# Kernel optimization log

Measured on AMD Instinct MI355X. Metric: run time of the kernel, lower is better.

The kernel has to match this reference:

```python
import jax, jax.numpy as jnp
import numpy as np

B, S, D = 4, 512, 4096
H, G = 32, 8           # num_heads, num_groups (GQA)
HD = D // H            # head_dim = 128
REP = H // G           # query heads per kv group = 4


def rotate_half(x):
    x1, x2 = x[..., : x.shape[-1] // 2], x[..., x.shape[-1] // 2 :]
    return jnp.concatenate([-x2, x1], axis=-1)


def setup_inputs() -> dict:
    key = jax.random.key(0)
    ks = jax.random.split(key, 5)
    return {
        "x": jax.random.normal(ks[0], (B, S, D), dtype=jnp.float32),
        "wq": jax.random.normal(ks[1], (D, D), dtype=jnp.float32) * 0.02,
        "bq": jnp.zeros((D,), dtype=jnp.float32),
        "wk": jax.random.normal(ks[2], (D, G * HD), dtype=jnp.float32) * 0.02,
        "bk": jnp.zeros((G * HD,), dtype=jnp.float32),
        "wv": jax.random.normal(ks[3], (D, G * HD), dtype=jnp.float32) * 0.02,
        "bv": jnp.zeros((G * HD,), dtype=jnp.float32),
        "wo": jax.random.normal(ks[4], (D, D), dtype=jnp.float32) * 0.02,
        "bo": jnp.zeros((D,), dtype=jnp.float32),
    }


def reference(x, wq, bq, wk, bk, wv, bv, wo, bo):
    b, s, d = x.shape
    q = (x @ wq + bq).reshape(b, s, H, HD)
    k = (x @ wk + bk).reshape(b, s, G, HD)
    v = (x @ wv + bv).reshape(b, s, G, HD)

    # RoPE tables (identical to module's cached sin/cos, sliced to seq len)
    inv_freq = 1.0 / (10000.0 ** (jnp.arange(0, HD, 2, dtype=jnp.float32) / HD))
    freqs = jnp.outer(jnp.arange(s, dtype=jnp.float32), inv_freq)  # [s, HD/2]
    freqs = jnp.concatenate([freqs, freqs], axis=-1)               # [s, HD]
    sin = jnp.sin(freqs)[:, None, :]  # [s, 1, HD] broadcast over heads
    cos = jnp.cos(freqs)[:, None, :]

    q = q * cos + rotate_half(q) * sin
    k = k * cos + rotate_half(k) * sin

    # Module scales q by HD**-0.5 AND jax.nn.dot_product_attention applies its
    # own default 1/sqrt(HD) -> net logit scale is HD**-1. Reproduce exactly.
    scale = HD ** (-0.5)
    q = q * scale

    # GQA without materializing repeated k/v: group query heads.
    qg = q.reshape(b, s, G, REP, HD)
    logits = jnp.einsum("bqgrd,bkgd->bgrqk", qg, k) * scale  # second scale (SDPA default)
    attn = jax.nn.softmax(logits, axis=-1)
    out = jnp.einsum("bgrqk,bkgd->bqgrd", attn, v).reshape(b, s, d)
    return out @ wo + bo
```

## Files before the change

### kernel.cpp

```cpp
#include <hip/hip_runtime.h>
#include <math.h>

typedef unsigned short ushort_t;
typedef __attribute__((ext_vector_type(8))) short bf16x8;
typedef __attribute__((ext_vector_type(4))) float f32x4;
typedef __attribute__((ext_vector_type(4))) unsigned short us4;
typedef __attribute__((ext_vector_type(8))) unsigned short us8;

#define B_   4
#define S_   512
#define D_   4096
#define H_   32
#define G_   8
#define HD_  128
#define KV_  1024
#define M_   (B_ * S_)
#define QN_  6144

__device__ __forceinline__ float bf2f(ushort_t u) {
    union { unsigned u; float f; } x; x.u = ((unsigned)u) << 16; return x.f;
}
__device__ __forceinline__ ushort_t f2bf(float f) {
    union { float f; unsigned u; } x; x.f = f;
    unsigned r = x.u + 0x7fffu + ((x.u >> 16) & 1u);
    return (ushort_t)(r >> 16);
}

typedef const __attribute__((address_space(1))) void* gptr_t;
typedef __attribute__((address_space(3))) void* ldsptr_t;

__device__ __forceinline__ void gload_lds16(const void* g, void* lds) {
    __builtin_amdgcn_global_load_lds((gptr_t)g, (ldsptr_t)lds, 16, 0, 0);
}

#define BAR() asm volatile("s_barrier" ::: "memory")
#define LGKM0() do { asm volatile("s_waitcnt lgkmcnt(0)" ::: "memory"); \
                     __builtin_amdgcn_sched_barrier(0); } while (0)

__global__ void xconv(const float* __restrict__ x, ushort_t* __restrict__ xb, int n8)
{
    const int i = blockIdx.x * blockDim.x + threadIdx.x;
    if (i >= n8) return;
    const float4 a = *(const float4*)&x[(size_t)i * 8];
    const float4 b = *(const float4*)&x[(size_t)i * 8 + 4];
    us8 o;
    o[0] = f2bf(a.x); o[1] = f2bf(a.y); o[2] = f2bf(a.z); o[3] = f2bf(a.w);
    o[4] = f2bf(b.x); o[5] = f2bf(b.y); o[6] = f2bf(b.z); o[7] = f2bf(b.w);
    *(us8*)&xb[(size_t)i * 8] = o;
}

__global__ __launch_bounds__(256) void wconv_all(
    const float* __restrict__ wq, const float* __restrict__ wk,
    const float* __restrict__ wv, ushort_t* __restrict__ Wt)
{
    __shared__ float t[32][33];
    const int n0 = blockIdx.x * 32, k0 = blockIdx.y * 32;
    const float* W; int nsrc, N;
    if (n0 < 4096)      { W = wq; nsrc = n0;        N = 4096; }
    else if (n0 < 5120) { W = wk; nsrc = n0 - 4096; N = 1024; }
    else                { W = wv; nsrc = n0 - 5120; N = 1024; }
    const int tid = threadIdx.x;
    const int r = tid >> 3, c4 = (tid & 7) * 4;
    const float4 v = *(const float4*)&W[(size_t)(k0 + r) * N + nsrc + c4];
    t[r][c4 + 0] = v.x; t[r][c4 + 1] = v.y; t[r][c4 + 2] = v.z; t[r][c4 + 3] = v.w;
    __syncthreads();
    us4 o;
    o.x = f2bf(t[c4 + 0][r]);
    o.y = f2bf(t[c4 + 1][r]);
    o.z = f2bf(t[c4 + 2][r]);
    o.w = f2bf(t[c4 + 3][r]);
    *(us4*)&Wt[(size_t)(n0 + r) * D_ + k0 + c4] = o;
}

__global__ __launch_bounds__(256) void wconv(
    const float* __restrict__ W, ushort_t* __restrict__ Wt, int K, int N)
{
    __shared__ float t[32][33];
    const int n0 = blockIdx.x * 32, k0 = blockIdx.y * 32;
    const int tid = threadIdx.x;
    const int r = tid >> 3, c4 = (tid & 7) * 4;
    const float4 v = *(const float4*)&W[(size_t)(k0 + r) * N + n0 + c4];
    t[r][c4 + 0] = v.x; t[r][c4 + 1] = v.y; t[r][c4 + 2] = v.z; t[r][c4 + 3] = v.w;
    __syncthreads();
    us4 o;
    o.x = f2bf(t[c4 + 0][r]);
    o.y = f2bf(t[c4 + 1][r]);
    o.z = f2bf(t[c4 + 2][r]);
    o.w = f2bf(t[c4 + 3][r]);
    *(us4*)&Wt[(size_t)(n0 + r) * K + k0 + c4] = o;
}

template<int OUT_BF16, int SPLITK, int ROPE>
__global__ __launch_bounds__(512, 2) void gemm8(
    const ushort_t* __restrict__ A, int lda,
    const ushort_t* __restrict__ Bt, int ldb,
    const float* __restrict__ bias0, const float* __restrict__ bias1,
    const float* __restrict__ bias2,
    float* __restrict__ Cf, ushort_t* __restrict__ Cb,
    float* __restrict__ P0, float* __restrict__ P1,
    int M, int N, int K)
{
    __shared__ ushort_t sA[2][256 * 64];
    __shared__ ushort_t sB[2][256 * 64];

    const int tid = threadIdx.x;
    const int lane = tid & 63, w = tid >> 6;
    const int lr = lane & 15, kg = lane >> 4;
    const int wr = w >> 2, wc = w & 3;

    const int nwg = gridDim.x;
    const int cpx = nwg >> 3;
    const int bid = (blockIdx.x & 7) * cpx + (blockIdx.x >> 3);
    int khalf = 0, tile = bid;
    if (SPLITK) { khalf = bid >> 7; tile = bid & 127; }
    const int nbx = N >> 8;
    const int bx = tile % nbx, by = tile / nbx;
    const int bm0 = by << 8, bn0 = bx << 8;
    if (SPLITK) { A += (size_t)khalf * K; Bt += (size_t)khalf * K; }

    const int NT = K >> 6;

    auto stage = [&](int t, int h) {
        const int c = t & 1;
        const ushort_t* gb; int ld; char* sbase;
        if (h < 2) { gb = A + (size_t)bm0 * lda; ld = lda; sbase = (char*)sA; }
        else       { gb = Bt + (size_t)bn0 * ldb; ld = ldb; sbase = (char*)sB; }
        const int half = h & 1;
        #pragma unroll
        for (int j = 0; j < 2; ++j) {
            const int o = j * 8192 + tid * 16;
            const int row = half * 128 + (o >> 7);
            const int slot = (o >> 4) & 7;
            gload_lds16(gb + (size_t)row * ld + t * 64 + ((slot ^ (row & 7)) << 3),
                        sbase + c * 32768 + half * 16384 + j * 8192 + w * 1024);
        }
    };
    auto lda_frag = [&](int c, int mi, int s) {
        const int row = mi * 32 + wr * 16 + lr;
        return *(const bf16x8*)((const char*)sA + c * 32768 + row * 128 +
                                (((s * 4 + kg) ^ (row & 7)) << 4));
    };
    auto ldb_frag = [&](int c, int ni, int s) {
        const int row = ni * 64 + wc * 16 + lr;
        return *(const bf16x8*)((const char*)sB + c * 32768 + row * 128 +
                                (((s * 4 + kg) ^ (row & 7)) << 4));
    };

    f32x4 acc[8][4];
    #pragma unroll
    for (int i = 0; i < 8; ++i)
        #pragma unroll
        for (int j = 0; j < 4; ++j)
            acc[i][j] = (f32x4){0.f, 0.f, 0.f, 0.f};

    stage(0, 0); stage(0, 2); stage(0, 3); stage(0, 1);
    stage(1, 0); stage(1, 2); stage(1, 3);
    asm volatile("s_waitcnt vmcnt(6)" ::: "memory");
    BAR();

    for (int t = 0; t < NT; ++t) {
        const int c = t & 1;
        bf16x8 a[4][2], b[4][2];

        #pragma unroll
        for (int mi = 0; mi < 4; ++mi)
            #pragma unroll
            for (int s = 0; s < 2; ++s) a[mi][s] = lda_frag(c, mi, s);
        #pragma unroll
        for (int ni = 0; ni < 2; ++ni)
            #pragma unroll
            for (int s = 0; s < 2; ++s) b[ni][s] = ldb_frag(c, ni, s);
        if (t + 1 < NT) stage(t + 1, 1);
        BAR();
        LGKM0();
        __builtin_amdgcn_s_setprio(1);
        #pragma unroll
        for (int mi = 0; mi < 4; ++mi)
            #pragma unroll
            for (int ni = 0; ni < 2; ++ni)
                #pragma unroll
                for (int s = 0; s < 2; ++s)
                    acc[mi][ni] = __builtin_amdgcn_mfma_f32_16x16x32_bf16(
                        a[mi][s], b[ni][s], acc[mi][ni], 0, 0, 0);
        __builtin_amdgcn_s_setprio(0);
        BAR();

        #pragma unroll
        for (int ni = 2; ni < 4; ++ni)
            #pragma unroll
            for (int s = 0; s < 2; ++s) b[ni][s] = ldb_frag(c, ni, s);
        if (t + 2 < NT) stage(t + 2, 0);
        BAR();
        LGKM0();
        __builtin_amdgcn_s_setprio(1);
        #pragma unroll
        for (int mi = 0; mi < 4; ++mi)
            #pragma unroll
            for (int ni = 2; ni < 4; ++ni)
                #pragma unroll
                for (int s = 0; s < 2; ++s)
                    acc[mi][ni] = __builtin_amdgcn_mfma_f32_16x16x32_bf16(
                        a[mi][s], b[ni][s], acc[mi][ni], 0, 0, 0);
        __builtin_amdgcn_s_setprio(0);
        BAR();

        #pragma unroll
        for (int mi = 0; mi < 4; ++mi)
            #pragma unroll
            for (int s = 0; s < 2; ++s) a[mi][s] = lda_frag(c, mi + 4, s);
        if (t + 2 < NT) stage(t + 2, 2);
        BAR();
        LGKM0();
        __builtin_amdgcn_s_setprio(1);
        #pragma unroll
        for (int mi = 0; mi < 4; ++mi)
            #pragma unroll
            for (int ni = 2; ni < 4; ++ni)
                #pragma unroll
                for (int s = 0; s < 2; ++s)
                    acc[mi + 4][ni] = __builtin_amdgcn_mfma_f32_16x16x32_bf16(
                        a[mi][s], b[ni][s], acc[mi + 4][ni], 0, 0, 0);
        __builtin_amdgcn_s_setprio(0);
        BAR();

        if (t + 2 < NT) {
            stage(t + 2, 3);
            asm volatile("s_waitcnt vmcnt(6)" ::: "memory");
        } else {
            asm volatile("s_waitcnt vmcnt(0)" ::: "memory");
        }
        BAR();
        __builtin_amdgcn_s_setprio(1);
        #pragma unroll
        for (int mi = 0; mi < 4; ++mi)
            #pragma unroll
            for (int ni = 0; ni < 2; ++ni)
                #pragma unroll
                for (int s = 0; s < 2; ++s)
                    acc[mi + 4][ni] = __builtin_amdgcn_mfma_f32_16x16x32_bf16(
                        a[mi][s], b[ni][s], acc[mi + 4][ni], 0, 0, 0);
        __builtin_amdgcn_s_setprio(0);
        BAR();
    }

    if (ROPE && bn0 < 5120) {
        const float scale = (bn0 < 4096) ? (1.f / 128.f) : 1.f;
        const int jj = wc * 16 + lr;
        const float invf = __expf(-0.1439115683121279f * (float)jj);
        #pragma unroll
        for (int mi = 0; mi < 8; ++mi) {
            const int mr = bm0 + mi * 32 + wr * 16 + kg * 4;
            #pragma unroll
            for (int r = 0; r < 4; ++r) {
                const int srow = (mr + r) & 511;
                float sn, cs;
                __sincosf((float)srow * invf, &sn, &cs);
                #pragma unroll
                for (int nip = 0; nip < 2; ++nip) {
                    const int n_lo = bn0 + nip * 128 + jj;
                    const int n_hi = n_lo + 64;
                    const float b_lo = (n_lo < 4096) ? bias0[n_lo]
                                     : (n_lo < 5120) ? bias1[n_lo - 4096] : bias2[n_lo - 5120];
                    const float b_hi = (n_hi < 4096) ? bias0[n_hi]
                                     : (n_hi < 5120) ? bias1[n_hi - 4096] : bias2[n_hi - 5120];
                    const float a_lo = acc[mi][nip * 2][r] + b_lo;
                    const float a_hi = acc[mi][nip * 2 + 1][r] + b_hi;
                    Cb[(size_t)(mr + r) * N + n_lo] = f2bf((a_lo * cs - a_hi * sn) * scale);
                    Cb[(size_t)(mr + r) * N + n_hi] = f2bf((a_hi * cs + a_lo * sn) * scale);
                }
            }
        }
        return;
    }
    #pragma unroll
    for (int mi = 0; mi < 8; ++mi) {
        #pragma unroll
        for (int ni = 0; ni < 4; ++ni) {
            const int n = bn0 + ni * 64 + wc * 16 + lr;
            const float bs = (n < 4096) ? bias0[n]
                           : (n < 5120) ? bias1[n - 4096] : bias2[n - 5120];
            const int mr = bm0 + mi * 32 + wr * 16 + kg * 4;
            #pragma unroll
            for (int r = 0; r < 4; ++r) {
                if (SPLITK) {
                    const int row = mr + r;
                    if (khalf == 0) {
                        Cf[(size_t)row * N + n] = acc[mi][ni][r] + bs;
                    } else {
                        float* P = (row < 1024) ? P0 : P1;
                        P[((size_t)(row & 1023) << 12) + n] = acc[mi][ni][r];
                    }
                } else {
                    const float val = acc[mi][ni][r] + bs;
                    if (OUT_BF16) Cb[(size_t)(mr + r) * N + n] = f2bf(val);
                    else          Cf[(size_t)(mr + r) * N + n] = val;
                }
            }
        }
    }
}

__global__ void reduce_add(const float* __restrict__ P0, const float* __restrict__ P1,
                           float* __restrict__ out)
{
    const int n4 = M_ * D_ / 4;
    for (int i4 = blockIdx.x * blockDim.x + threadIdx.x; i4 < n4;
         i4 += gridDim.x * blockDim.x) {
        const float4 p = (i4 < (1 << 20))
            ? *(const float4*)&P0[(size_t)i4 * 4]
            : *(const float4*)&P1[(size_t)(i4 - (1 << 20)) * 4];
        float4 o = *(float4*)&out[(size_t)i4 * 4];
        o.x += p.x; o.y += p.y; o.z += p.z; o.w += p.w;
        *(float4*)&out[(size_t)i4 * 4] = o;
    }
}

__global__ __launch_bounds__(256) void vtrans(
    const ushort_t* __restrict__ vb,
    ushort_t* __restrict__ vT)
{
    __shared__ ushort_t t[32][40];
    const int s0 = blockIdx.x * 32;
    const int d0 = blockIdx.y * 32;
    const int bg = blockIdx.z;
    const int b = bg >> 3, g = bg & 7;
    const int tid = threadIdx.x;
    const int row = tid >> 3, c4 = (tid & 7) * 4;
    const us4 v = *(const us4*)&vb[(size_t)(b * S_ + s0 + row) * QN_ + g * HD_ + d0 + c4];
    t[row][c4 + 0] = v.x; t[row][c4 + 1] = v.y;
    t[row][c4 + 2] = v.z; t[row][c4 + 3] = v.w;
    __syncthreads();
    us4 o;
    o.x = t[c4 + 0][row]; o.y = t[c4 + 1][row];
    o.z = t[c4 + 2][row]; o.w = t[c4 + 3][row];
    *(us4*)&vT[(size_t)(bg * HD_ + d0 + row) * S_ + s0 + c4] = o;
}

__global__ __launch_bounds__(256) void attn_mfma(
    const ushort_t* __restrict__ kb,
    const ushort_t* __restrict__ vT,
    ushort_t* __restrict__ qb)
{
    __shared__ ushort_t sKV[8192];
    __shared__ ushort_t sP[4 * 16 * 512];

    const int q0 = blockIdx.x * 64;
    const int h = blockIdx.y, b = blockIdx.z;
    const int g = h >> 2;
    const int tid = threadIdx.x;
    const int lane = tid & 63, w = tid >> 6;
    const int lr = lane & 15, kg = lane >> 4;

    bf16x8 af[4];
    {
        const ushort_t* qrow = qb + (size_t)(b * S_ + q0 + w * 16 + lr) * QN_ + h * HD_;
        #pragma unroll
        for (int c = 0; c < 4; ++c)
            af[c] = *(const bf16x8*)(qrow + c * 32 + kg * 8);
    }

    f32x4 l[8][4];
    #pragma unroll
    for (int ch = 0; ch < 8; ++ch)
        #pragma unroll
        for (int t = 0; t < 4; ++t)
            l[ch][t] = (f32x4){0.f, 0.f, 0.f, 0.f};

    const ushort_t* kbase = kb + (size_t)b * S_ * QN_ + g * HD_;
    #pragma unroll
    for (int ch = 0; ch < 8; ++ch) {
        __syncthreads();
        #pragma unroll
        for (int i = 0; i < 4; ++i) {
            const int o = w * 4096 + i * 1024;
            const int key = (o >> 8) + (lane >> 4);
            const int sl = lane & 15;
            gload_lds16(kbase + (size_t)(ch * 64 + key) * QN_ + ((sl ^ (key & 15)) * 8),
                        (char*)sKV + o);
        }
        __syncthreads();
        #pragma unroll
        for (int t = 0; t < 4; ++t) {
            const int key = t * 16 + lr;
            #pragma unroll
            for (int c = 0; c < 4; ++c) {
                const bf16x8 bf = *(const bf16x8*)((const char*)sKV + key * 256 +
                                                   (((c * 4 + kg) ^ (key & 15)) << 4));
                l[ch][t] = __builtin_amdgcn_mfma_f32_16x16x32_bf16(af[c], bf, l[ch][t], 0, 0, 0);
            }
        }
    }

    float inv[4];
    #pragma unroll
    for (int r = 0; r < 4; ++r) {
        float m = -1e30f;
        #pragma unroll
        for (int ch = 0; ch < 8; ++ch)
            #pragma unroll
            for (int t = 0; t < 4; ++t)
                m = fmaxf(m, l[ch][t][r]);
        #pragma unroll
        for (int msk = 1; msk <= 8; msk <<= 1)
            m = fmaxf(m, __shfl_xor(m, msk));
        float s = 0.f;
        const int q = kg * 4 + r;
        #pragma unroll
        for (int ch = 0; ch < 8; ++ch)
            #pragma unroll
            for (int t = 0; t < 4; ++t) {
                const float p = __expf(l[ch][t][r] - m);
                s += p;
                const int gs = ch * 8 + t * 2 + (lr >> 3);
                sP[w * 8192 + q * 512 + ((gs ^ q) << 3) + (lr & 7)] = f2bf(p);
            }
        #pragma unroll
        for (int msk = 1; msk <= 8; msk <<= 1)
            s += __shfl_xor(s, msk);
        inv[r] = 1.f / s;
    }

    f32x4 oacc[8];
    #pragma unroll
    for (int dt = 0; dt < 8; ++dt) oacc[dt] = (f32x4){0.f, 0.f, 0.f, 0.f};

    const ushort_t* vbase = vT + (size_t)(b * G_ + g) * HD_ * S_;
    for (int ch = 0; ch < 8; ++ch) {
        __syncthreads();
        #pragma unroll
        for (int i = 0; i < 4; ++i) {
            const int o = w * 4096 + i * 1024;
            const int d = (o >> 7) + (lane >> 3);
            const int sl = lane & 7;
            gload_lds16(vbase + (size_t)d * S_ + ch * 64 + ((sl ^ (d & 7)) * 8),
                        (char*)sKV + o);
        }
        __syncthreads();
        #pragma unroll
        for (int c2 = 0; c2 < 2; ++c2) {
            const int gs = ch * 8 + c2 * 4 + kg;
            const bf16x8 ap = *(const bf16x8*)((const char*)sP + w * 16384 + lr * 1024 +
                                               ((gs ^ lr) << 4));
            #pragma unroll
            for (int dt = 0; dt < 8; ++dt) {
                const int d = dt * 16 + lr;
                const bf16x8 bv = *(const bf16x8*)((const char*)sKV + d * 128 +
                                                   (((c2 * 4 + kg) ^ (d & 7)) << 4));
                oacc[dt] = __builtin_amdgcn_mfma_f32_16x16x32_bf16(ap, bv, oacc[dt], 0, 0, 0);
            }
        }
    }

    #pragma unroll
    for (int dt = 0; dt < 8; ++dt) {
        #pragma unroll
        for (int r = 0; r < 4; ++r) {
            const int q = kg * 4 + r;
            qb[(size_t)(b * S_ + q0 + w * 16 + q) * QN_ + h * HD_ + dt * 16 + lr] =
                f2bf(oacc[dt][r] * inv[r]);
        }
    }
}

extern "C" void kernel_launch(void* const* d_in, const int* in_sizes, int n_in,
                              void* d_out, int out_size, void* d_ws, size_t ws_size,
                              hipStream_t stream)
{
    const float* x  = (const float*)d_in[0];
    const float* wq = (const float*)d_in[1];
    const float* bq = (const float*)d_in[2];
    const float* wk = (const float*)d_in[3];
    const float* bk = (const float*)d_in[4];
    const float* wv = (const float*)d_in[5];
    const float* bv = (const float*)d_in[6];
    const float* wo = (const float*)d_in[7];
    const float* bo = (const float*)d_in[8];
    float* out = (float*)d_out;

    char* ws = (char*)d_ws;
    ushort_t* xb   = (ushort_t*)(ws);
    ushort_t* Wt   = (ushort_t*)(ws + (16u << 20));
    ushort_t* vT   = (ushort_t*)(ws + (48u << 20));
    ushort_t* qkv  = (ushort_t*)(ws + (64u << 20));
    float* p0      = (float*)xb;
    float* p1      = (float*)(ws + (48u << 20));

    wconv_all<<<dim3(QN_ / 32, D_ / 32), 256, 0, stream>>>(wq, wk, wv, Wt);
    xconv<<<(M_ * D_ / 8 + 255) / 256, 256, 0, stream>>>(x, xb, M_ * D_ / 8);

    gemm8<1, 0, 1><<<(QN_ / 256) * (M_ / 256), 512, 0, stream>>>(
        xb, D_, Wt, D_, bq, bk, bv, nullptr, qkv, nullptr, nullptr, M_, QN_, D_);

    vtrans<<<dim3(S_ / 32, HD_ / 32, B_ * G_), 256, 0, stream>>>(qkv + 5120, vT);

    attn_mfma<<<dim3(S_ / 64, H_, B_), 256, 0, stream>>>(qkv + 4096, vT, qkv);

    wconv<<<dim3(D_ / 32, D_ / 32), 256, 0, stream>>>(wo, Wt, D_, D_);

    gemm8<0, 1, 0><<<256, 512, 0, stream>>>(
        qkv, QN_, Wt, D_, bo, bo, bo, out, nullptr, p0, p1, M_, D_, 2048);
    reduce_add<<<2048, 256, 0, stream>>>(p0, p1, out);
}
```

Before: 311.3 us.

## Fuse split-K reduction into GEMM via ticket handoff and drop explicit LDS waits

The output projection GEMM now reduces its two K-halves in-kernel. The first block to finish a tile writes its partials and releases a flag; the second block spins on the flag, adds the partials with the bias and writes the output. This removes the separate reduce_add launch and its extra full-size read/write traffic, at the cost of a spin-wait that depends on both blocks being resident. Separately, the explicit lgkmcnt(0) waits and sched_barriers are removed and the fragment load order is swapped, letting the compiler schedule LDS waits more finely.

After: 447.5 us. 1.44x slower.

```diff
diff --git a/kernel.cpp b/kernel.cpp
--- a/kernel.cpp
+++ b/kernel.cpp
@@ -34,8 +34,6 @@
 }
 
 #define BAR() asm volatile("s_barrier" ::: "memory")
-#define LGKM0() do { asm volatile("s_waitcnt lgkmcnt(0)" ::: "memory"); \
-                     __builtin_amdgcn_sched_barrier(0); } while (0)
 
 __global__ void xconv(const float* __restrict__ x, ushort_t* __restrict__ xb, int n8)
 {
@@ -98,7 +96,7 @@
     const float* __restrict__ bias2,
     float* __restrict__ Cf, ushort_t* __restrict__ Cb,
     float* __restrict__ P0, float* __restrict__ P1,
-    int M, int N, int K)
+    int M, int N, int K, int* tickets)
 {
     __shared__ ushort_t sA[2][256 * 64];
     __shared__ ushort_t sB[2][256 * 64];
@@ -163,16 +161,15 @@
         bf16x8 a[4][2], b[4][2];
 
         #pragma unroll
+        for (int ni = 0; ni < 2; ++ni)
+            #pragma unroll
+            for (int s = 0; s < 2; ++s) b[ni][s] = ldb_frag(c, ni, s);
+        #pragma unroll
         for (int mi = 0; mi < 4; ++mi)
             #pragma unroll
             for (int s = 0; s < 2; ++s) a[mi][s] = lda_frag(c, mi, s);
-        #pragma unroll
-        for (int ni = 0; ni < 2; ++ni)
-            #pragma unroll
-            for (int s = 0; s < 2; ++s) b[ni][s] = ldb_frag(c, ni, s);
         if (t + 1 < NT) stage(t + 1, 1);
         BAR();
-        LGKM0();
         __builtin_amdgcn_s_setprio(1);
         #pragma unroll
         for (int mi = 0; mi < 4; ++mi)
@@ -191,7 +188,6 @@
             for (int s = 0; s < 2; ++s) b[ni][s] = ldb_frag(c, ni, s);
         if (t + 2 < NT) stage(t + 2, 0);
         BAR();
-        LGKM0();
         __builtin_amdgcn_s_setprio(1);
         #pragma unroll
         for (int mi = 0; mi < 4; ++mi)
@@ -210,7 +206,6 @@
             for (int s = 0; s < 2; ++s) a[mi][s] = lda_frag(c, mi + 4, s);
         if (t + 2 < NT) stage(t + 2, 2);
         BAR();
-        LGKM0();
         __builtin_amdgcn_s_setprio(1);
         #pragma unroll
         for (int mi = 0; mi < 4; ++mi)
@@ -269,6 +264,52 @@
                     Cb[(size_t)(mr + r) * N + n_hi] = f2bf((a_hi * cs + a_lo * sn) * scale);
                 }
             }
+        }
+        return;
+    }
+    if (SPLITK && tickets) {
+        float* P = (tile < 64) ? (P0 + (size_t)tile * 65536)
+                               : (P1 + (size_t)(tile - 64) * 65536);
+        int* tk = tickets + tile * 2;
+        __shared__ int role_sh;
+        if (tid == 0) role_sh = atomicAdd(&tk[0], 1);
+        __syncthreads();
+        if (role_sh == 0) {
+            #pragma unroll
+            for (int mi = 0; mi < 8; ++mi)
+                #pragma unroll
+                for (int ni = 0; ni < 4; ++ni) {
+                    const int lcol = ni * 64 + wc * 16 + lr;
+                    const int lrow = mi * 32 + wr * 16 + kg * 4;
+                    #pragma unroll
+                    for (int r = 0; r < 4; ++r)
+                        P[(lrow + r) * 256 + lcol] = acc[mi][ni][r];
+                }
+            __threadfence();
+            __syncthreads();
+            if (tid == 0)
+                __hip_atomic_store(&tk[1], 1, __ATOMIC_RELEASE, __HIP_MEMORY_SCOPE_AGENT);
+        } else {
+            if (tid == 0)
+                while (__hip_atomic_load(&tk[1], __ATOMIC_ACQUIRE,
+                                         __HIP_MEMORY_SCOPE_AGENT) == 0)
+                    __builtin_amdgcn_s_sleep(8);
+            __syncthreads();
+            __threadfence();
+            #pragma unroll
+            for (int mi = 0; mi < 8; ++mi)
+                #pragma unroll
+                for (int ni = 0; ni < 4; ++ni) {
+                    const int lcol = ni * 64 + wc * 16 + lr;
+                    const int n = bn0 + lcol;
+                    const float bs = bias0[n];
+                    const int lrow = mi * 32 + wr * 16 + kg * 4;
+                    const int mr = bm0 + lrow;
+                    #pragma unroll
+                    for (int r = 0; r < 4; ++r)
+                        Cf[(size_t)(mr + r) * N + n] =
+                            (acc[mi][ni][r] + P[(lrow + r) * 256 + lcol]) + bs;
+                }
         }
         return;
     }
@@ -485,11 +526,15 @@
     float* p0      = (float*)xb;
     float* p1      = (float*)(ws + (48u << 20));
 
+    const bool use_ticket = (ws_size >= ((88ull << 20) + 1024));
+    int* tickets = (int*)(ws + (88ull << 20));
+    if (use_ticket) hipMemsetAsync(tickets, 0, 1024, stream);
+
     wconv_all<<<dim3(QN_ / 32, D_ / 32), 256, 0, stream>>>(wq, wk, wv, Wt);
     xconv<<<(M_ * D_ / 8 + 255) / 256, 256, 0, stream>>>(x, xb, M_ * D_ / 8);
 
     gemm8<1, 0, 1><<<(QN_ / 256) * (M_ / 256), 512, 0, stream>>>(
-        xb, D_, Wt, D_, bq, bk, bv, nullptr, qkv, nullptr, nullptr, M_, QN_, D_);
+        xb, D_, Wt, D_, bq, bk, bv, nullptr, qkv, nullptr, nullptr, M_, QN_, D_, nullptr);
 
     vtrans<<<dim3(S_ / 32, HD_ / 32, B_ * G_), 256, 0, stream>>>(qkv + 5120, vT);
 
@@ -498,6 +543,8 @@
     wconv<<<dim3(D_ / 32, D_ / 32), 256, 0, stream>>>(wo, Wt, D_, D_);
 
     gemm8<0, 1, 0><<<256, 512, 0, stream>>>(
-        qkv, QN_, Wt, D_, bo, bo, bo, out, nullptr, p0, p1, M_, D_, 2048);
-    reduce_add<<<2048, 256, 0, stream>>>(p0, p1, out);
-}
+        qkv, QN_, Wt, D_, bo, bo, bo, out, nullptr, p0, p1, M_, D_, 2048,
+        use_ticket ? tickets : nullptr);
+    if (!use_ticket)
+        reduce_add<<<2048, 256, 0, stream>>>(p0, p1, out);
+}
```
